# Performance work log

Measured on AMD Instinct MI355X. Metric: run time of the kernel, lower is better.

## Reference

```python
import jax, jax.numpy as jnp
import numpy as np
import math

N_NODES = 25000
N_EDGES = 400000
FEAT = 128
N_RBF = 20
CUTOFF = 5.0
EPS = 1e-15


def setup_inputs() -> dict:
    key = jax.random.key(0)
    ks = jax.random.split(key, 10)
    s_j = jax.random.normal(ks[0], (N_NODES, FEAT), dtype=jnp.float32)
    v_j = jax.random.normal(ks[1], (N_NODES, FEAT, 3), dtype=jnp.float32)
    r_ij = jax.random.normal(ks[2], (N_EDGES, 3), dtype=jnp.float32)
    nbrs = jax.random.randint(ks[3], (N_EDGES, 2), 0, N_NODES, dtype=jnp.int64)
    # InvariantDense: Linear(F,F) -> swish -> Linear(F,3F)
    sc1 = 1.0 / math.sqrt(FEAT)
    W1 = jax.random.uniform(ks[4], (FEAT, FEAT), jnp.float32, -sc1, sc1)
    b1 = jnp.zeros((FEAT,), jnp.float32)
    W2 = jax.random.uniform(ks[5], (FEAT, 3 * FEAT), jnp.float32, -sc1, sc1)
    b2 = jnp.zeros((3 * FEAT,), jnp.float32)
    # DistanceEmbed dense: Linear(n_rbf, 3F)
    scd = 1.0 / math.sqrt(N_RBF)
    Wd = jax.random.uniform(ks[6], (N_RBF, 3 * FEAT), jnp.float32, -scd, scd)
    bd = jnp.zeros((3 * FEAT,), jnp.float32)
    return {"s_j": s_j, "v_j": v_j, "r_ij": r_ij, "nbrs": nbrs,
            "W1": W1, "b1": b1, "W2": W2, "b2": b2, "Wd": Wd, "bd": bd}


def _swish(x):
    return x * jax.nn.sigmoid(x)


def reference(s_j, v_j, r_ij, nbrs, W1, b1, W2, b2, Wd, bd):
    # preprocess_r
    dist = jnp.sqrt(jnp.sum(r_ij * r_ij + EPS, axis=-1))        # [E]
    unit = r_ij / dist[:, None]                                  # [E, 3]

    src = nbrs[:, 1]
    dst = nbrs[:, 0]

    # invariant dense on gathered scalar features
    s_nb = s_j[src]                                              # [E, F]
    phi = _swish(s_nb @ W1 + b1) @ W2 + b2                       # [E, 3F]

    # radial basis: sin(n*pi*d/cutoff)/d, n = 1..n_rbf
    n = jnp.arange(1, N_RBF + 1, dtype=jnp.float32)
    rbf = jnp.sin(n * jnp.pi / CUTOFF * dist[:, None]) / dist[:, None]  # [E, n_rbf]
    w_s = rbf @ Wd + bd                                          # [E, 3F]

    inv = (phi * w_s).reshape(-1, FEAT, 3)                       # [E, F, 3]
    split0 = inv[:, :, 0:1]                                      # [E, F, 1]
    split1 = inv[:, :, 1]                                        # [E, F]
    split2 = inv[:, :, 2:3]                                      # [E, F, 1]

    delta_v_ij = split2 * unit[:, None, :] + split0 * v_j[src]   # [E, F, 3]
    delta_s_ij = split1                                          # [E, F]

    delta_s_i = jax.ops.segment_sum(delta_s_ij, dst, num_segments=s_j.shape[0])
    delta_v_i = jax.ops.segment_sum(delta_v_ij, dst, num_segments=s_j.shape[0])
    return (delta_s_i, delta_v_i)
```

## Files before the change

### kernel.cpp

```cpp
#include <hip/hip_runtime.h>

namespace {

constexpr int FEAT   = 128;
constexpr int NRBF   = 20;
constexpr int EPB    = 32;
constexpr int NNODES = 25000;
constexpr int NEDGES = 400000;
constexpr int NBLK   = NEDGES / EPB;
constexpr float PI_F = 3.14159265358979323846f;

using f32x4 = __attribute__((ext_vector_type(4))) float;
using s16x8 = __attribute__((ext_vector_type(8))) short;
using s16x4 = __attribute__((ext_vector_type(4))) short;

constexpr int PW1_ELEMS = 8  * 4 * 64 * 8;
constexpr int PW2_ELEMS = 24 * 4 * 64 * 8;
constexpr int PWD_ELEMS = 24 * 1 * 64 * 8;
constexpr int PW1_OFF = 0;
constexpr int PW2_OFF = PW1_ELEMS;
constexpr int PWD_OFF = PW1_ELEMS + PW2_ELEMS;
constexpr int PT_TOTAL = PW1_ELEMS + PW2_ELEMS + PWD_ELEMS;

__device__ inline unsigned short f2bf(float f) {
    unsigned u = __builtin_bit_cast(unsigned, f);
    u += 0x7fffu + ((u >> 16) & 1u);
    return (unsigned short)(u >> 16);
}
__device__ inline float bf2f(unsigned short h) {
    unsigned u = ((unsigned)h) << 16;
    return __builtin_bit_cast(float, u);
}

__global__ __launch_bounds__(256) void prep_kernel(
    const float* __restrict__ W1, const float* __restrict__ W2,
    const float* __restrict__ Wd, short* __restrict__ pw)
{
    const int idx = blockIdx.x * 256 + threadIdx.x;
    if (idx >= PT_TOTAL) return;
    float val;
    if (idx < PW2_OFF) {
        const int t = idx;
        const int r = t & 7, lane = (t >> 3) & 63, ks = (t >> 9) & 3, nt = t >> 11;
        const int k = ks*32 + (lane>>4)*8 + r, n = nt*16 + (lane & 15);
        val = W1[k*128 + n];
    } else if (idx < PWD_OFF) {
        const int t = idx - PW2_OFF;
        const int r = t & 7, lane = (t >> 3) & 63, ks = (t >> 9) & 3, nt = t >> 11;
        const int k = ks*32 + (lane>>4)*8 + r, n = nt*16 + (lane & 15);
        val = W2[k*384 + n];
    } else {
        const int t = idx - PWD_OFF;
        const int r = t & 7, lane = (t >> 3) & 63, nt = t >> 9;
        const int k = (lane>>4)*8 + r, n = nt*16 + (lane & 15);
        val = (k < NRBF) ? Wd[k*384 + n] : 0.f;
    }
    pw[idx] = (short)f2bf(val);
}

__global__ __launch_bounds__(256) void hist_kernel(
    const int* __restrict__ nbrs, int* __restrict__ hist)
{
    const int e = blockIdx.x * 256 + threadIdx.x;
    if (e >= NEDGES) return;
    atomicAdd(&hist[nbrs[2*e]], 1);
}

__global__ __launch_bounds__(256) void scan_kernel(
    const int* __restrict__ hist, int* __restrict__ cursor)
{
    __shared__ int part[256];
    const int t = threadIdx.x;
    constexpr int CH = (NNODES + 255) / 256;
    const int base = t * CH;
    int s = 0;
    for (int i = 0; i < CH; ++i) {
        const int idx = base + i;
        if (idx < NNODES) s += hist[idx];
    }
    part[t] = s;
    __syncthreads();
    for (int off = 1; off < 256; off <<= 1) {
        int v = part[t];
        if (t >= off) v += part[t - off];
        __syncthreads();
        part[t] = v;
        __syncthreads();
    }
    int run = part[t] - s;
    for (int i = 0; i < CH; ++i) {
        const int idx = base + i;
        if (idx < NNODES) { cursor[idx] = run; run += hist[idx]; }
    }
}

__global__ __launch_bounds__(256) void scatter_kernel(
    const int* __restrict__ nbrs, int* __restrict__ cursor,
    int* __restrict__ eids)
{
    const int e = blockIdx.x * 256 + threadIdx.x;
    if (e >= NEDGES) return;
    const int dst = nbrs[2*e];
    const int pos = atomicAdd(&cursor[dst], 1);
    eids[pos] = e;
}

__global__ __launch_bounds__(256) void msg_kernel(
    const float* __restrict__ s_j, const float* __restrict__ v_j,
    const float* __restrict__ r_ij, const int* __restrict__ nbrs,
    const float* __restrict__ b1, const float* __restrict__ b2,
    const float* __restrict__ bd, const short* __restrict__ pw,
    const int* __restrict__ eids,
    float* __restrict__ ds_out, float* __restrict__ dv_out)
{
    __shared__ short sA[EPB * 128];
    __shared__ short sH[EPB * 128];
    __shared__ short sR[EPB * 64];
    __shared__ short sI[EPB * 384];
    __shared__ float sU[EPB][3];
    __shared__ int   sSrc[EPB], sDst[EPB];

    const int tid = threadIdx.x;
    const int w   = tid >> 6;
    const int l   = tid & 63;
    const int mr  = l & 15;
    const int g   = l >> 4;
    const int e0  = blockIdx.x * EPB;

    if (tid < EPB) {
        const int eid = eids[e0 + tid];
        sDst[tid] = nbrs[2*eid + 0];
        sSrc[tid] = nbrs[2*eid + 1];
        const float r0 = r_ij[3*eid+0], r1 = r_ij[3*eid+1], r2 = r_ij[3*eid+2];
        const float d     = sqrtf(r0*r0 + r1*r1 + r2*r2 + 3e-15f);
        const float inv_d = 1.0f / d;
        sU[tid][0] = r0*inv_d; sU[tid][1] = r1*inv_d; sU[tid][2] = r2*inv_d;
        const int xr = (tid & 7) << 3;
        #pragma unroll
        for (int k = 0; k < 64; ++k) {
            const float v = (k < NRBF) ? __sinf((float)(k+1)*(PI_F/5.0f)*d)*inv_d : 0.f;
            sR[tid*64 + (k ^ xr)] = (short)f2bf(v);
        }
    }

    #pragma unroll
    for (int p = 0; p < 4; ++p) {
        const int v  = tid + p*256;
        const int e  = v >> 5;
        const int c4 = (v & 31) * 4;
        const int eid = eids[e0 + e];
        const int src = nbrs[2*eid + 1];
        const float4 f = reinterpret_cast<const float4*>(s_j + (size_t)src*FEAT)[v & 31];
        s16x4 h;
        h.x = (short)f2bf(f.x); h.y = (short)f2bf(f.y);
        h.z = (short)f2bf(f.z); h.w = (short)f2bf(f.w);
        *reinterpret_cast<s16x4*>(&sA[e*128 + (c4 ^ ((e & 7) << 3))]) = h;
    }
    __syncthreads();

    {
        s16x8 aS[2][4];
        #pragma unroll
        for (int mt = 0; mt < 2; ++mt) {
            const int m = mt*16 + mr;
            const int xr = (m & 7) << 3;
            #pragma unroll
            for (int ks = 0; ks < 4; ++ks)
                aS[mt][ks] = *reinterpret_cast<const s16x8*>(&sA[m*128 + ((ks*32 + g*8) ^ xr)]);
        }
        const s16x8* pW1 = reinterpret_cast<const s16x8*>(pw + PW1_OFF);
        #pragma unroll
        for (int i = 0; i < 2; ++i) {
            const int nt = w*2 + i;
            const int n  = nt*16 + mr;
            const float b1n = b1[n];
            f32x4 acc[2] = {f32x4{0,0,0,0}, f32x4{0,0,0,0}};
            #pragma unroll
            for (int ks = 0; ks < 4; ++ks) {
                const s16x8 b = pW1[(nt*4 + ks)*64 + l];
                acc[0] = __builtin_amdgcn_mfma_f32_16x16x32_bf16(aS[0][ks], b, acc[0], 0, 0, 0);
                acc[1] = __builtin_amdgcn_mfma_f32_16x16x32_bf16(aS[1][ks], b, acc[1], 0, 0, 0);
            }
            #pragma unroll
            for (int mt = 0; mt < 2; ++mt)
                #pragma unroll
                for (int r = 0; r < 4; ++r) {
                    const int m = mt*16 + g*4 + r;
                    const float x = acc[mt][r] + b1n;
                    const float hsw = x / (1.0f + __expf(-x));
                    sH[m*128 + (n ^ ((m & 7) << 3))] = (short)f2bf(hsw);
                }
        }
    }
    __syncthreads();

    {
        s16x8 aH[2][4], aR[2];
        #pragma unroll
        for (int mt = 0; mt < 2; ++mt) {
            const int m = mt*16 + mr;
            const int xr = (m & 7) << 3;
            #pragma unroll
            for (int ks = 0; ks < 4; ++ks)
                aH[mt][ks] = *reinterpret_cast<const s16x8*>(&sH[m*128 + ((ks*32 + g*8) ^ xr)]);
            aR[mt] = *reinterpret_cast<const s16x8*>(&sR[m*64 + ((g*8) ^ xr)]);
        }
        const s16x8* pW2 = reinterpret_cast<const s16x8*>(pw + PW2_OFF);
        const s16x8* pWd = reinterpret_cast<const s16x8*>(pw + PWD_OFF);
        #pragma unroll
        for (int i = 0; i < 6; ++i) {
            const int nt = w*6 + i;
            const int n  = nt*16 + mr;
            const float b2n = b2[n], bdn = bd[n];
            f32x4 acc[2]  = {f32x4{0,0,0,0}, f32x4{0,0,0,0}};
            f32x4 accw[2] = {f32x4{0,0,0,0}, f32x4{0,0,0,0}};
            #pragma unroll
            for (int ks = 0; ks < 4; ++ks) {
                const s16x8 b = pW2[(nt*4 + ks)*64 + l];
                acc[0] = __builtin_amdgcn_mfma_f32_16x16x32_bf16(aH[0][ks], b, acc[0], 0, 0, 0);
                acc[1] = __builtin_amdgcn_mfma_f32_16x16x32_bf16(aH[1][ks], b, acc[1], 0, 0, 0);
            }
            const s16x8 bw = pWd[nt*64 + l];
            accw[0] = __builtin_amdgcn_mfma_f32_16x16x32_bf16(aR[0], bw, accw[0], 0, 0, 0);
            accw[1] = __builtin_amdgcn_mfma_f32_16x16x32_bf16(aR[1], bw, accw[1], 0, 0, 0);
            #pragma unroll
            for (int mt = 0; mt < 2; ++mt)
                #pragma unroll
                for (int r = 0; r < 4; ++r) {
                    const int m = mt*16 + g*4 + r;
                    const float inv = (acc[mt][r] + b2n) * (accw[mt][r] + bdn);
                    sI[m*384 + n] = (short)f2bf(inv);
                }
        }
    }
    __syncthreads();

    {
        const int half = tid >> 7;
        const int f    = tid & 127;
        const int eb   = half * 16;
        float accS = 0.f, a0 = 0.f, a1 = 0.f, a2 = 0.f;
        int cur = sDst[eb];
        #pragma unroll 4
        for (int e = eb; e < eb + 16; ++e) {
            const int d = sDst[e];
            if (d != cur) {
                atomicAdd(ds_out + (size_t)cur*FEAT + f, accS);
                float* dvp = dv_out + (size_t)cur*(3*FEAT) + 3*f;
                atomicAdd(dvp + 0, a0);
                atomicAdd(dvp + 1, a1);
                atomicAdd(dvp + 2, a2);
                accS = a0 = a1 = a2 = 0.f;
                cur = d;
            }
            const float i0 = bf2f((unsigned short)sI[e*384 + 3*f + 0]);
            const float i1 = bf2f((unsigned short)sI[e*384 + 3*f + 1]);
            const float i2 = bf2f((unsigned short)sI[e*384 + 3*f + 2]);
            const int src = sSrc[e];
            const float* vj = v_j + (size_t)src*(3*FEAT) + 3*f;
            const float u0 = sU[e][0], u1 = sU[e][1], u2 = sU[e][2];
            accS += i1;
            a0 += i2*u0 + i0*vj[0];
            a1 += i2*u1 + i0*vj[1];
            a2 += i2*u2 + i0*vj[2];
        }
        atomicAdd(ds_out + (size_t)cur*FEAT + f, accS);
        float* dvp = dv_out + (size_t)cur*(3*FEAT) + 3*f;
        atomicAdd(dvp + 0, a0);
        atomicAdd(dvp + 1, a1);
        atomicAdd(dvp + 2, a2);
    }
}

}

extern "C" void kernel_launch(void* const* d_in, const int* in_sizes, int n_in,
                              void* d_out, int out_size, void* d_ws, size_t ws_size,
                              hipStream_t stream)
{
    const float* s_j  = (const float*)d_in[0];
    const float* v_j  = (const float*)d_in[1];
    const float* r_ij = (const float*)d_in[2];
    const int*   nbrs = (const int*)d_in[3];
    const float* W1   = (const float*)d_in[4];
    const float* b1   = (const float*)d_in[5];
    const float* W2   = (const float*)d_in[6];
    const float* b2   = (const float*)d_in[7];
    const float* Wd   = (const float*)d_in[8];
    const float* bd   = (const float*)d_in[9];

    float* ds_out = (float*)d_out;
    float* dv_out = ds_out + (size_t)NNODES * FEAT;

    char* base   = (char*)d_ws;
    short* pw    = (short*)base;
    int*  hist   = (int*)(base + 160*1024);
    int*  cursor = (int*)(base + 272*1024);
    int*  eids   = (int*)(base + 384*1024);

    hipMemsetAsync(d_out, 0, (size_t)out_size * sizeof(float), stream);
    hipMemsetAsync(hist, 0, NNODES * sizeof(int), stream);

    prep_kernel<<<(PT_TOTAL + 255)/256, 256, 0, stream>>>(W1, W2, Wd, pw);
    hist_kernel<<<(NEDGES + 255)/256, 256, 0, stream>>>(nbrs, hist);
    scan_kernel<<<1, 256, 0, stream>>>(hist, cursor);
    scatter_kernel<<<(NEDGES + 255)/256, 256, 0, stream>>>(nbrs, cursor, eids);

    msg_kernel<<<NBLK, 256, 0, stream>>>(
        s_j, v_j, r_ij, nbrs, b1, b2, bd, pw, eids, ds_out, dv_out);
}
```

Measured before the change: 486.4 us.

## Parallelize scan, permute W2 columns into planar layout, reuse shared tile

Replaces the single-block serial prefix scan with a three-kernel multi-block scan, so the histogram offsets no longer wait on one workgroup. Permutes W2/Wd columns in prep so the per-edge products come out as three planar feature arrays, stored with XOR swizzle into a shared tile that overlaps the earlier A/H/R buffers. This cuts LDS use (better occupancy) and avoids strided bank-conflicting reads in the scatter phase. It also spreads the RBF computation across all 256 threads instead of 32, with vectorized LDS stores. The cost is an extra barrier in stage two and two extra kernel launches.

```diff
diff --git a/kernel.cpp b/kernel.cpp
--- a/kernel.cpp
+++ b/kernel.cpp
@@ -8,6 +8,7 @@
 constexpr int NNODES = 25000;
 constexpr int NEDGES = 400000;
 constexpr int NBLK   = NEDGES / EPB;
+constexpr int NSCAN  = (NNODES + 255) / 256;
 constexpr float PI_F = 3.14159265358979323846f;
 
 using f32x4 = __attribute__((ext_vector_type(4))) float;
@@ -48,12 +49,14 @@
         const int t = idx - PW2_OFF;
         const int r = t & 7, lane = (t >> 3) & 63, ks = (t >> 9) & 3, nt = t >> 11;
         const int k = ks*32 + (lane>>4)*8 + r, n = nt*16 + (lane & 15);
-        val = W2[k*384 + n];
+        const int orig = 3*(n & 127) + (n >> 7);
+        val = W2[k*384 + orig];
     } else {
         const int t = idx - PWD_OFF;
         const int r = t & 7, lane = (t >> 3) & 63, nt = t >> 9;
         const int k = (lane>>4)*8 + r, n = nt*16 + (lane & 15);
-        val = (k < NRBF) ? Wd[k*384 + n] : 0.f;
+        const int orig = 3*(n & 127) + (n >> 7);
+        val = (k < NRBF) ? Wd[k*384 + orig] : 0.f;
     }
     pw[idx] = (short)f2bf(val);
 }
@@ -63,35 +66,50 @@
 {
     const int e = blockIdx.x * 256 + threadIdx.x;
     if (e >= NEDGES) return;
-    atomicAdd(&hist[nbrs[2*e]], 1);
-}
-
-__global__ __launch_bounds__(256) void scan_kernel(
-    const int* __restrict__ hist, int* __restrict__ cursor)
-{
-    __shared__ int part[256];
+    const int2 nb = reinterpret_cast<const int2*>(nbrs)[e];
+    atomicAdd(&hist[nb.x], 1);
+}
+
+__global__ __launch_bounds__(256) void scanA_kernel(
+    const int* __restrict__ hist, int* __restrict__ cursor, int* __restrict__ bsum)
+{
+    __shared__ int sh[256];
+    const int t = threadIdx.x, idx = blockIdx.x*256 + t;
+    const int v = (idx < NNODES) ? hist[idx] : 0;
+    sh[t] = v; __syncthreads();
+    int acc = v;
+    for (int off = 1; off < 256; off <<= 1) {
+        const int add = (t >= off) ? sh[t-off] : 0;
+        __syncthreads();
+        acc += add; sh[t] = acc;
+        __syncthreads();
+    }
+    if (idx < NNODES) cursor[idx] = acc - v;
+    if (t == 255) bsum[blockIdx.x] = acc;
+}
+
+__global__ __launch_bounds__(128) void scanB_kernel(
+    const int* __restrict__ bsum, int* __restrict__ boffs)
+{
+    __shared__ int sh[128];
     const int t = threadIdx.x;
-    constexpr int CH = (NNODES + 255) / 256;
-    const int base = t * CH;
-    int s = 0;
-    for (int i = 0; i < CH; ++i) {
-        const int idx = base + i;
-        if (idx < NNODES) s += hist[idx];
-    }
-    part[t] = s;
-    __syncthreads();
-    for (int off = 1; off < 256; off <<= 1) {
-        int v = part[t];
-        if (t >= off) v += part[t - off];
-        __syncthreads();
-        part[t] = v;
-        __syncthreads();
-    }
-    int run = part[t] - s;
-    for (int i = 0; i < CH; ++i) {
-        const int idx = base + i;
-        if (idx < NNODES) { cursor[idx] = run; run += hist[idx]; }
-    }
+    const int v = (t < NSCAN) ? bsum[t] : 0;
+    sh[t] = v; __syncthreads();
+    int acc = v;
+    for (int off = 1; off < 128; off <<= 1) {
+        const int add = (t >= off) ? sh[t-off] : 0;
+        __syncthreads();
+        acc += add; sh[t] = acc;
+        __syncthreads();
+    }
+    if (t < NSCAN) boffs[t] = acc - v;
+}
+
+__global__ __launch_bounds__(256) void scanC_kernel(
+    int* __restrict__ cursor, const int* __restrict__ boffs)
+{
+    const int idx = blockIdx.x*256 + threadIdx.x;
+    if (idx < NNODES) cursor[idx] += boffs[blockIdx.x];
 }
 
 __global__ __launch_bounds__(256) void scatter_kernel(
@@ -113,12 +131,10 @@
     const int* __restrict__ eids,
     float* __restrict__ ds_out, float* __restrict__ dv_out)
 {
-    __shared__ short sA[EPB * 128];
-    __shared__ short sH[EPB * 128];
-    __shared__ short sR[EPB * 64];
-    __shared__ short sI[EPB * 384];
+    __shared__ short sTile[12288];
     __shared__ float sU[EPB][3];
     __shared__ int   sSrc[EPB], sDst[EPB];
+    constexpr int OFF_A = 0, OFF_H = 4096, OFF_R = 8192;
 
     const int tid = threadIdx.x;
     const int w   = tid >> 6;
@@ -127,20 +143,26 @@
     const int g   = l >> 4;
     const int e0  = blockIdx.x * EPB;
 
-    if (tid < EPB) {
-        const int eid = eids[e0 + tid];
-        sDst[tid] = nbrs[2*eid + 0];
-        sSrc[tid] = nbrs[2*eid + 1];
+    {
+        const int ep  = tid >> 3;
+        const int sub = tid & 7;
+        const int eid = eids[e0 + ep];
+        const int2 nb = reinterpret_cast<const int2*>(nbrs)[eid];
         const float r0 = r_ij[3*eid+0], r1 = r_ij[3*eid+1], r2 = r_ij[3*eid+2];
         const float d     = sqrtf(r0*r0 + r1*r1 + r2*r2 + 3e-15f);
         const float inv_d = 1.0f / d;
-        sU[tid][0] = r0*inv_d; sU[tid][1] = r1*inv_d; sU[tid][2] = r2*inv_d;
-        const int xr = (tid & 7) << 3;
-        #pragma unroll
-        for (int k = 0; k < 64; ++k) {
+        if (sub == 0) {
+            sDst[ep] = nb.x; sSrc[ep] = nb.y;
+            sU[ep][0] = r0*inv_d; sU[ep][1] = r1*inv_d; sU[ep][2] = r2*inv_d;
+        }
+        s16x8 rv;
+        #pragma unroll
+        for (int kk = 0; kk < 8; ++kk) {
+            const int k = sub*8 + kk;
             const float v = (k < NRBF) ? __sinf((float)(k+1)*(PI_F/5.0f)*d)*inv_d : 0.f;
-            sR[tid*64 + (k ^ xr)] = (short)f2bf(v);
-        }
+            rv[kk] = (short)f2bf(v);
+        }
+        *reinterpret_cast<s16x8*>(&sTile[OFF_R + ep*64 + ((sub*8) ^ ((ep & 7) << 3))]) = rv;
     }
 
     #pragma unroll
@@ -154,7 +176,7 @@
         s16x4 h;
         h.x = (short)f2bf(f.x); h.y = (short)f2bf(f.y);
         h.z = (short)f2bf(f.z); h.w = (short)f2bf(f.w);
-        *reinterpret_cast<s16x4*>(&sA[e*128 + (c4 ^ ((e & 7) << 3))]) = h;
+        *reinterpret_cast<s16x4*>(&sTile[OFF_A + e*128 + (c4 ^ ((e & 7) << 3))]) = h;
     }
     __syncthreads();
 
@@ -166,7 +188,7 @@
             const int xr = (m & 7) << 3;
             #pragma unroll
             for (int ks = 0; ks < 4; ++ks)
-                aS[mt][ks] = *reinterpret_cast<const s16x8*>(&sA[m*128 + ((ks*32 + g*8) ^ xr)]);
+                aS[mt][ks] = *reinterpret_cast<const s16x8*>(&sTile[OFF_A + m*128 + ((ks*32 + g*8) ^ xr)]);
         }
         const s16x8* pW1 = reinterpret_cast<const s16x8*>(pw + PW1_OFF);
         #pragma unroll
@@ -188,7 +210,7 @@
                     const int m = mt*16 + g*4 + r;
                     const float x = acc[mt][r] + b1n;
                     const float hsw = x / (1.0f + __expf(-x));
-                    sH[m*128 + (n ^ ((m & 7) << 3))] = (short)f2bf(hsw);
+                    sTile[OFF_H + m*128 + (n ^ ((m & 7) << 3))] = (short)f2bf(hsw);
                 }
         }
     }
@@ -202,16 +224,21 @@
             const int xr = (m & 7) << 3;
             #pragma unroll
             for (int ks = 0; ks < 4; ++ks)
-                aH[mt][ks] = *reinterpret_cast<const s16x8*>(&sH[m*128 + ((ks*32 + g*8) ^ xr)]);
-            aR[mt] = *reinterpret_cast<const s16x8*>(&sR[m*64 + ((g*8) ^ xr)]);
-        }
+                aH[mt][ks] = *reinterpret_cast<const s16x8*>(&sTile[OFF_H + m*128 + ((ks*32 + g*8) ^ xr)]);
+            aR[mt] = *reinterpret_cast<const s16x8*>(&sTile[OFF_R + m*64 + ((g*8) ^ xr)]);
+        }
+        __syncthreads();
+
         const s16x8* pW2 = reinterpret_cast<const s16x8*>(pw + PW2_OFF);
         const s16x8* pWd = reinterpret_cast<const s16x8*>(pw + PWD_OFF);
         #pragma unroll
         for (int i = 0; i < 6; ++i) {
             const int nt = w*6 + i;
             const int n  = nt*16 + mr;
-            const float b2n = b2[n], bdn = bd[n];
+            const int c  = n >> 7;
+            const int f2 = n & 127;
+            const int orig = 3*f2 + c;
+            const float b2n = b2[orig], bdn = bd[orig];
             f32x4 acc[2]  = {f32x4{0,0,0,0}, f32x4{0,0,0,0}};
             f32x4 accw[2] = {f32x4{0,0,0,0}, f32x4{0,0,0,0}};
             #pragma unroll
@@ -229,7 +256,7 @@
                 for (int r = 0; r < 4; ++r) {
                     const int m = mt*16 + g*4 + r;
                     const float inv = (acc[mt][r] + b2n) * (accw[mt][r] + bdn);
-                    sI[m*384 + n] = (short)f2bf(inv);
+                    sTile[c*4096 + m*128 + (f2 ^ ((m & 7) << 3))] = (short)f2bf(inv);
                 }
         }
     }
@@ -253,9 +280,10 @@
                 accS = a0 = a1 = a2 = 0.f;
                 cur = d;
             }
-            const float i0 = bf2f((unsigned short)sI[e*384 + 3*f + 0]);
-            const float i1 = bf2f((unsigned short)sI[e*384 + 3*f + 1]);
-            const float i2 = bf2f((unsigned short)sI[e*384 + 3*f + 2]);
+            const int fx = f ^ ((e & 7) << 3);
+            const float i0 = bf2f((unsigned short)sTile[        e*128 + fx]);
+            const float i1 = bf2f((unsigned short)sTile[4096 + e*128 + fx]);
+            const float i2 = bf2f((unsigned short)sTile[8192 + e*128 + fx]);
             const int src = sSrc[e];
             const float* vj = v_j + (size_t)src*(3*FEAT) + 3*f;
             const float u0 = sU[e][0], u1 = sU[e][1], u2 = sU[e][2];
@@ -296,6 +324,8 @@
     short* pw    = (short*)base;
     int*  hist   = (int*)(base + 160*1024);
     int*  cursor = (int*)(base + 272*1024);
+    int*  bsum   = (int*)(base + 376*1024);
+    int*  boffs  = (int*)(base + 380*1024);
     int*  eids   = (int*)(base + 384*1024);
 
     hipMemsetAsync(d_out, 0, (size_t)out_size * sizeof(float), stream);
@@ -303,7 +333,9 @@
 
     prep_kernel<<<(PT_TOTAL + 255)/256, 256, 0, stream>>>(W1, W2, Wd, pw);
     hist_kernel<<<(NEDGES + 255)/256, 256, 0, stream>>>(nbrs, hist);
-    scan_kernel<<<1, 256, 0, stream>>>(hist, cursor);
+    scanA_kernel<<<NSCAN, 256, 0, stream>>>(hist, cursor, bsum);
+    scanB_kernel<<<1, 128, 0, stream>>>(bsum, boffs);
+    scanC_kernel<<<NSCAN, 256, 0, stream>>>(cursor, boffs);
     scatter_kernel<<<(NEDGES + 255)/256, 256, 0, stream>>>(nbrs, cursor, eids);
 
     msg_kernel<<<NBLK, 256, 0, stream>>>(
```

Result: faster. 438.2 us (-9.9%).
